# Optimization experiments

Measured on AMD Instinct MI355X. Metric: run time of the kernel, lower is better.

The kernel has to match this reference:

```python
import jax, jax.numpy as jnp
import numpy as np

N = 100          # num_objects
H = 128          # decoder_hidden
D = 128          # input_size (== H, required by the module's GRU linears)
REL = 7          # num_relative_features (use_3d=False)
E = N * (N - 1)  # fully-connected, no self loops
B = 32

_mask = ~np.eye(N, dtype=bool)
_SEND_NP, _RECV_NP = np.where(_mask)  # torch.where(~eye): rows=send, cols=recv
SEND = jnp.asarray(_SEND_NP, dtype=jnp.int32)
RECV = jnp.asarray(_RECV_NP, dtype=jnp.int32)


def setup_inputs() -> dict:
    key = jax.random.key(0)
    ks = jax.random.split(key, 34)
    def w(k, shape, scale=0.05):
        return jax.random.normal(k, shape, dtype=jnp.float32) * scale
    inp = {
        "inputs": jax.random.normal(ks[0], (B, N, D), jnp.float32),
        "edge_attr": jax.random.normal(ks[1], (B, E, REL + D), jnp.float32),
        "hidden": jax.random.normal(ks[2], (B, N, H), jnp.float32),
        # msg_mlp: Linear(2H,H) Tanh Linear(H,H) Tanh
        "msg_w1": w(ks[3], (2 * H, H)), "msg_b1": w(ks[4], (H,)),
        "msg_w2": w(ks[5], (H, H)),     "msg_b2": w(ks[6], (H,)),
        # present_msg_mlp: Linear(REL+D,H) ReLU Linear(H,H) ReLU
        "pm_w1": w(ks[7], (REL + D, H)), "pm_b1": w(ks[8], (H,)),
        "pm_w2": w(ks[9], (H, H)),       "pm_b2": w(ks[10], (H,)),
        # res_mlp: Linear(D,H) ReLU Linear(H,H) ReLU
        "res_w1": w(ks[11], (D, H)), "res_b1": w(ks[12], (H,)),
        "res_w2": w(ks[13], (H, H)), "res_b2": w(ks[14], (H,)),
        # GRU-style gates
        "ir_w": w(ks[15], (H, H)), "ir_b": w(ks[16], (H,)),
        "ii_w": w(ks[17], (H, H)), "ii_b": w(ks[18], (H,)),
        "in_w": w(ks[19], (H, H)), "in_b": w(ks[20], (H,)),
        "hr_w": w(ks[21], (H, H)),
        "hi_w": w(ks[22], (H, H)),
        "hh_w": w(ks[23], (H, H)),
        # out_mlp: Linear(H,H) ReLU Linear(H,H) ReLU Linear(H,D)
        "out_w1": w(ks[24], (H, H)), "out_b1": w(ks[25], (H,)),
        "out_w2": w(ks[26], (H, H)), "out_b2": w(ks[27], (H,)),
        "out_w3": w(ks[28], (H, D)), "out_b3": w(ks[29], (D,)),
    }
    return inp


def _scatter_mean(msgs, recv, num_nodes):
    # msgs: [B, E, H] -> [B, N, H], mean over incoming edges per node
    counts = jnp.zeros((num_nodes,), msgs.dtype).at[recv].add(1.0)
    summed = jnp.zeros((msgs.shape[0], num_nodes, msgs.shape[-1]), msgs.dtype)
    summed = summed.at[:, recv].add(msgs)
    return summed / counts[None, :, None]


def reference(inputs, edge_attr, hidden,
              msg_w1, msg_b1, msg_w2, msg_b2,
              pm_w1, pm_b1, pm_w2, pm_b2,
              res_w1, res_b1, res_w2, res_b2,
              ir_w, ir_b, ii_w, ii_b, in_w, in_b,
              hr_w, hi_w, hh_w,
              out_w1, out_b1, out_w2, out_b2, out_w3, out_b3):
    # gather hidden states along edges (dropout is identity: p=0 / eval)
    hm = jnp.concatenate([hidden[:, RECV], hidden[:, SEND]], axis=-1)  # [B,E,2H]
    hm = jnp.tanh(jnp.tanh(hm @ msg_w1 + msg_b1) @ msg_w2 + msg_b2)
    hidden_node = _scatter_mean(hm, RECV, N)                           # [B,N,H]

    pm = jax.nn.relu(jax.nn.relu(edge_attr @ pm_w1 + pm_b1) @ pm_w2 + pm_b2)
    present_node = _scatter_mean(pm, RECV, N)
    present_node = present_node + jax.nn.relu(
        jax.nn.relu(inputs @ res_w1 + res_b1) @ res_w2 + res_b2)

    r = jax.nn.sigmoid(present_node @ ir_w + ir_b + hidden_node @ hr_w)
    i = jax.nn.sigmoid(present_node @ ii_w + ii_b + hidden_node @ hi_w)
    n = jnp.tanh(present_node @ in_w + in_b + r * (hidden_node @ hh_w))
    hidden_new = (1.0 - i) * n + i * hidden

    pred = jax.nn.relu(hidden_new @ out_w1 + out_b1)
    pred = jax.nn.relu(pred @ out_w2 + out_b2)
    pred = pred @ out_w3 + out_b3
    return pred, hidden_new
```

## Files before the change

### kernel.cpp

```cpp
#include <hip/hip_runtime.h>

typedef unsigned short u16;
typedef unsigned int   u32;
typedef __attribute__((ext_vector_type(8))) short bf8;
typedef __attribute__((ext_vector_type(4))) float f4;

#define DF __device__ __forceinline__

DF float bf2f(u16 h){ u32 u = ((u32)h) << 16; float f; __builtin_memcpy(&f, &u, 4); return f; }
DF u16 f2bf(float f){ u32 u; __builtin_memcpy(&u, &f, 4); u = (u + 0x7FFFu + ((u >> 16) & 1u)) >> 16; return (u16)u; }
DF float fexp2(float x){ return __builtin_amdgcn_exp2f(x); }
DF float frcp (float x){ return __builtin_amdgcn_rcpf(x); }
DF float tanhF(float x){ float e = fexp2(2.8853900817779268f * x); return 1.0f - 2.0f * frcp(e + 1.0f); }
DF float sigF (float x){ return frcp(1.0f + fexp2(-1.4426950408889634f * x)); }
DF float4 ld4u(const float* p){ float4 v; __builtin_memcpy(&v, p, 16); return v; }
DF u32 cvtpk(float lo, float hi){ u32 r; asm("v_cvt_pk_bf16_f32 %0, %1, %2" : "=v"(r) : "v"(lo), "v"(hi)); return r; }

DF const bf8* fragp(const u16* packed, int w, int nt, int ks, int lane){
  return reinterpret_cast<const bf8*>(packed + (((w * 32 + nt * 4 + ks) * 64 + lane) * 8));
}
DF const bf8* fragp_pm1(const u16* packed, int nt, int ks, int lane){
  return reinterpret_cast<const bf8*>(packed + (((512 + nt * 5 + ks) * 64 + lane) * 8));
}

struct WPtrs { const float* p[16]; };

__global__ __launch_bounds__(256) void k_pack(WPtrs wp, u16* __restrict__ packed){
  int bi = blockIdx.x;
  int lane = threadIdx.x & 63, warp = threadIdx.x >> 6;
  if(bi == 16){
    const float* __restrict__ src = wp.p[14];
    u16* __restrict__ dst = packed + 512 * 64 * 8;
    for(int i = warp; i < 40; i += 4){
      int nt = i / 5, ks = i - nt * 5;
      int col = nt * 16 + (lane & 15);
      int kb  = ks * 32 + (lane >> 4) * 8;
      u16* o = dst + (i * 64 + lane) * 8;
      for(int j = 0; j < 8; j++){
        int row = kb + j;
        o[j] = (row < 135) ? f2bf(src[row * 128 + col]) : (u16)0;
      }
    }
    return;
  }
  const float* __restrict__ src = wp.p[bi];
  u16* __restrict__ dst = packed + bi * 32 * 64 * 8;
  for(int i = warp; i < 32; i += 4){
    int nt = i >> 2, ks = i & 3;
    int col = nt * 16 + (lane & 15);
    int kb  = ks * 32 + (lane >> 4) * 8;
    u16* o = dst + (i * 64 + lane) * 8;
    for(int j = 0; j < 8; j++) o[j] = f2bf(src[(kb + j) * 128 + col]);
  }
}

__global__ __launch_bounds__(512) void k_node_pre(
    const float* __restrict__ hidden, const float* __restrict__ inputs,
    const u16* __restrict__ packed,
    const float* __restrict__ res_b1, const float* __restrict__ res_b2,
    float* __restrict__ Ptop, float* __restrict__ Pbot, float* __restrict__ res2)
{
  __shared__ __align__(16) u16 hid[64 * 136];
  __shared__ __align__(16) u16 inp[64 * 136];
  __shared__ __align__(16) u16 t1s[64 * 136];
  int row0 = blockIdx.x * 64;
  int t = threadIdx.x, lane = t & 63, w = t >> 6;
  int lrow = lane & 15, lk = lane >> 4;
  for(int i = t; i < 64 * 128; i += 512){
    int rr = i >> 7, cc = i & 127;
    hid[rr * 136 + cc] = f2bf(hidden[(row0 + rr) * 128 + cc]);
    inp[rr * 136 + cc] = f2bf(inputs[(row0 + rr) * 128 + cc]);
  }
  bf8 f0[4], f1[4], f5[4], f6[4];
  #pragma unroll
  for(int k = 0; k < 4; k++){
    f0[k] = *fragp(packed, 0, w, k, lane);
    f1[k] = *fragp(packed, 1, w, k, lane);
    f5[k] = *fragp(packed, 5, w, k, lane);
    f6[k] = *fragp(packed, 6, w, k, lane);
  }
  int col = w * 16 + lrow;
  float rb1 = res_b1[col], rb2 = res_b2[col];
  __syncthreads();
  #pragma unroll
  for(int m = 0; m < 4; m++){
    bf8 a[4], a2[4];
    #pragma unroll
    for(int k = 0; k < 4; k++){
      a[k]  = *reinterpret_cast<const bf8*>(&hid[(m * 16 + lrow) * 136 + k * 32 + lk * 8]);
      a2[k] = *reinterpret_cast<const bf8*>(&inp[(m * 16 + lrow) * 136 + k * 32 + lk * 8]);
    }
    f4 c0 = {0.f,0.f,0.f,0.f}, c1 = {0.f,0.f,0.f,0.f}, c2 = {0.f,0.f,0.f,0.f};
    #pragma unroll
    for(int k = 0; k < 4; k++){
      c0 = __builtin_amdgcn_mfma_f32_16x16x32_bf16(a[k],  f0[k], c0, 0, 0, 0);
      c1 = __builtin_amdgcn_mfma_f32_16x16x32_bf16(a[k],  f1[k], c1, 0, 0, 0);
      c2 = __builtin_amdgcn_mfma_f32_16x16x32_bf16(a2[k], f5[k], c2, 0, 0, 0);
    }
    #pragma unroll
    for(int q = 0; q < 4; q++){
      int gr = row0 + m * 16 + lk * 4 + q;
      Ptop[gr * 128 + col] = c0[q];
      Pbot[gr * 128 + col] = c1[q];
      float v = c2[q] + rb1; v = v > 0.f ? v : 0.f;
      t1s[(m * 16 + lk * 4 + q) * 136 + col] = f2bf(v);
    }
  }
  __syncthreads();
  #pragma unroll
  for(int m = 0; m < 4; m++){
    bf8 a3[4];
    #pragma unroll
    for(int k = 0; k < 4; k++)
      a3[k] = *reinterpret_cast<const bf8*>(&t1s[(m * 16 + lrow) * 136 + k * 32 + lk * 8]);
    f4 c = {0.f,0.f,0.f,0.f};
    #pragma unroll
    for(int k = 0; k < 4; k++)
      c = __builtin_amdgcn_mfma_f32_16x16x32_bf16(a3[k], f6[k], c, 0, 0, 0);
    #pragma unroll
    for(int q = 0; q < 4; q++){
      float v = c[q] + rb2; v = v > 0.f ? v : 0.f;
      res2[(row0 + m * 16 + lk * 4 + q) * 128 + col] = v;
    }
  }
}

__global__ __launch_bounds__(256, 4) void k_edge(
    const float* __restrict__ EA,
    const float* __restrict__ Ptop, const float* __restrict__ Pbot,
    const float* __restrict__ msg_b1, const float* __restrict__ msg_b2,
    const float* __restrict__ pm_b1, const float* __restrict__ pm_b2,
    const u16* __restrict__ packed,
    float* __restrict__ hnode, float* __restrict__ pnode)
{
  __shared__ __align__(16) u16 bufA[112 * 128];
  __shared__ __align__(16) u16 tail[112 * 8];
  char* bb = (char*)bufA;
  char* tb = (char*)tail;
  int blk = blockIdx.x;
  int b = blk / 100, r = blk - b * 100;
  int t = threadIdx.x, lane = t & 63, w = t >> 6;
  int lrow = lane & 15, lk = lane >> 4;
  int n0 = 2 * w, n1 = 2 * w + 1;

  {
    for(int i = t; i < 99 * 16; i += 256){
      int row = i >> 4, g = i & 15;
      int s = row + (row >= r ? 1 : 0);
      int e = s * 99 + (r < s ? r : r - 1);
      const float* rp = EA + ((size_t)(b * 9900 + e)) * 135 + g * 8;
      float4 v0 = ld4u(rp), v1 = ld4u(rp + 4);
      u32 pk[4] = {cvtpk(v0.x, v0.y), cvtpk(v0.z, v0.w), cvtpk(v1.x, v1.y), cvtpk(v1.z, v1.w)};
      *reinterpret_cast<uint4*>(bb + row * 256 + ((g ^ (row & 7)) << 4)) = *reinterpret_cast<const uint4*>(pk);
    }
    for(int row = t; row < 99; row += 256){
      int s = row + (row >= r ? 1 : 0);
      int e = s * 99 + (r < s ? r : r - 1);
      const float* rp = EA + ((size_t)(b * 9900 + e)) * 135 + 128;
      float4 v0 = ld4u(rp);
      u32 pk[4] = {cvtpk(v0.x, v0.y), cvtpk(v0.z, v0.w), cvtpk(rp[4], rp[5]), cvtpk(rp[6], 0.f)};
      *reinterpret_cast<uint4*>(tb + row * 16) = *reinterpret_cast<const uint4*>(pk);
    }
    bf8 w1a[5], w1b[5];
    #pragma unroll
    for(int k = 0; k < 5; k++){ w1a[k] = *fragp_pm1(packed, n0, k, lane); w1b[k] = *fragp_pm1(packed, n1, k, lane); }
    float b1a = pm_b1[n0 * 16 + lrow], b1b = pm_b1[n1 * 16 + lrow];
    __syncthreads();

    f4 cA0[4], cA1[4];
    #pragma unroll
    for(int m = 0; m < 4; m++){
      int arow = m * 16 + lrow, sw = arow & 7;
      bf8 a[4];
      #pragma unroll
      for(int k = 0; k < 4; k++)
        a[k] = *reinterpret_cast<const bf8*>(bb + arow * 256 + (((k * 4 + lk) ^ sw) << 4));
      bf8 a4 = {0,0,0,0,0,0,0,0};
      if(lk == 0) a4 = *reinterpret_cast<const bf8*>(tb + arow * 16);
      f4 c0 = {0.f,0.f,0.f,0.f}, c1 = {0.f,0.f,0.f,0.f};
      #pragma unroll
      for(int k = 0; k < 4; k++){
        c0 = __builtin_amdgcn_mfma_f32_16x16x32_bf16(a[k], w1a[k], c0, 0, 0, 0);
        c1 = __builtin_amdgcn_mfma_f32_16x16x32_bf16(a[k], w1b[k], c1, 0, 0, 0);
      }
      c0 = __builtin_amdgcn_mfma_f32_16x16x32_bf16(a4, w1a[4], c0, 0, 0, 0);
      c1 = __builtin_amdgcn_mfma_f32_16x16x32_bf16(a4, w1b[4], c1, 0, 0, 0);
      cA0[m] = c0; cA1[m] = c1;
    }
    __syncthreads();

    #pragma unroll
    for(int m = 0; m < 4; m++){
      #pragma unroll
      for(int qp = 0; qp < 2; qp++){
        float v0 = cA0[m][2*qp]   + b1a; v0 = v0 > 0.f ? v0 : 0.f;
        float u0 = cA0[m][2*qp+1] + b1a; u0 = u0 > 0.f ? u0 : 0.f;
        float v1 = cA1[m][2*qp]   + b1b; v1 = v1 > 0.f ? v1 : 0.f;
        float u1 = cA1[m][2*qp+1] + b1b; u1 = u1 > 0.f ? u1 : 0.f;
        u32 p0 = cvtpk(v0, u0), p1 = cvtpk(v1, u1);
        int row0_ = m * 16 + lk * 4 + 2 * qp;
        int sw0 = (row0_ & 7) << 4, sw1 = ((row0_ + 1) & 7) << 4;
        *reinterpret_cast<u16*>(bb + row0_ * 256       + (((n0 * 16 + lrow) * 2) ^ sw0)) = (u16)p0;
        *reinterpret_cast<u16*>(bb + (row0_ + 1) * 256 + (((n0 * 16 + lrow) * 2) ^ sw1)) = (u16)(p0 >> 16);
        *reinterpret_cast<u16*>(bb + row0_ * 256       + (((n1 * 16 + lrow) * 2) ^ sw0)) = (u16)p1;
        *reinterpret_cast<u16*>(bb + (row0_ + 1) * 256 + (((n1 * 16 + lrow) * 2) ^ sw1)) = (u16)(p1 >> 16);
      }
    }
    f4 cB0[3], cB1[3];
    #pragma unroll
    for(int m = 0; m < 3; m++){
      int arow = (m + 4) * 16 + lrow, sw = arow & 7;
      bf8 a[4];
      #pragma unroll
      for(int k = 0; k < 4; k++)
        a[k] = *reinterpret_cast<const bf8*>(bb + arow * 256 + (((k * 4 + lk) ^ sw) << 4));
      bf8 a4 = {0,0,0,0,0,0,0,0};
      if(lk == 0) a4 = *reinterpret_cast<const bf8*>(tb + arow * 16);
      f4 c0 = {0.f,0.f,0.f,0.f}, c1 = {0.f,0.f,0.f,0.f};
      #pragma unroll
      for(int k = 0; k < 4; k++){
        c0 = __builtin_amdgcn_mfma_f32_16x16x32_bf16(a[k], w1a[k], c0, 0, 0, 0);
        c1 = __builtin_amdgcn_mfma_f32_16x16x32_bf16(a[k], w1b[k], c1, 0, 0, 0);
      }
      c0 = __builtin_amdgcn_mfma_f32_16x16x32_bf16(a4, w1a[4], c0, 0, 0, 0);
      c1 = __builtin_amdgcn_mfma_f32_16x16x32_bf16(a4, w1b[4], c1, 0, 0, 0);
      cB0[m] = c0; cB1[m] = c1;
    }
    __syncthreads();

    #pragma unroll
    for(int m = 0; m < 3; m++){
      #pragma unroll
      for(int qp = 0; qp < 2; qp++){
        float v0 = cB0[m][2*qp]   + b1a; v0 = v0 > 0.f ? v0 : 0.f;
        float u0 = cB0[m][2*qp+1] + b1a; u0 = u0 > 0.f ? u0 : 0.f;
        float v1 = cB1[m][2*qp]   + b1b; v1 = v1 > 0.f ? v1 : 0.f;
        float u1 = cB1[m][2*qp+1] + b1b; u1 = u1 > 0.f ? u1 : 0.f;
        u32 p0 = cvtpk(v0, u0), p1 = cvtpk(v1, u1);
        int row0_ = (m + 4) * 16 + lk * 4 + 2 * qp;
        int sw0 = (row0_ & 7) << 4, sw1 = ((row0_ + 1) & 7) << 4;
        *reinterpret_cast<u16*>(bb + row0_ * 256       + (((n0 * 16 + lrow) * 2) ^ sw0)) = (u16)p0;
        *reinterpret_cast<u16*>(bb + (row0_ + 1) * 256 + (((n0 * 16 + lrow) * 2) ^ sw1)) = (u16)(p0 >> 16);
        *reinterpret_cast<u16*>(bb + row0_ * 256       + (((n1 * 16 + lrow) * 2) ^ sw0)) = (u16)p1;
        *reinterpret_cast<u16*>(bb + (row0_ + 1) * 256 + (((n1 * 16 + lrow) * 2) ^ sw1)) = (u16)(p1 >> 16);
      }
    }
    __syncthreads();

    bf8 w2a[4], w2b[4];
    #pragma unroll
    for(int k = 0; k < 4; k++){ w2a[k] = *fragp(packed, 15, n0, k, lane); w2b[k] = *fragp(packed, 15, n1, k, lane); }
    float b2a = pm_b2[n0 * 16 + lrow], b2b = pm_b2[n1 * 16 + lrow];
    float acc0 = 0.f, acc1 = 0.f;
    #pragma unroll
    for(int m = 0; m < 7; m++){
      int arow = m * 16 + lrow, sw = arow & 7;
      bf8 a[4];
      #pragma unroll
      for(int k = 0; k < 4; k++)
        a[k] = *reinterpret_cast<const bf8*>(bb + arow * 256 + (((k * 4 + lk) ^ sw) << 4));
      f4 c0 = {0.f,0.f,0.f,0.f}, c1 = {0.f,0.f,0.f,0.f};
      #pragma unroll
      for(int k = 0; k < 4; k++){
        c0 = __builtin_amdgcn_mfma_f32_16x16x32_bf16(a[k], w2a[k], c0, 0, 0, 0);
        c1 = __builtin_amdgcn_mfma_f32_16x16x32_bf16(a[k], w2b[k], c1, 0, 0, 0);
      }
      #pragma unroll
      for(int q = 0; q < 4; q++){
        int rr = m * 16 + lk * 4 + q;
        if(rr < 99){
          float v0 = c0[q] + b2a; acc0 += (v0 > 0.f ? v0 : 0.f);
          float v1 = c1[q] + b2b; acc1 += (v1 > 0.f ? v1 : 0.f);
        }
      }
    }
    acc0 += __shfl_xor(acc0, 16); acc0 += __shfl_xor(acc0, 32);
    acc1 += __shfl_xor(acc1, 16); acc1 += __shfl_xor(acc1, 32);
    if(lane < 16){
      float* dst = pnode + ((size_t)b * 100 + r) * 128;
      dst[n0 * 16 + lane] = acc0 * (1.0f / 99.0f);
      dst[n1 * 16 + lane] = acc1 * (1.0f / 99.0f);
    }
  }
  __syncthreads();

  {
    bf8 w2a[4], w2b[4];
    #pragma unroll
    for(int k = 0; k < 4; k++){ w2a[k] = *fragp(packed, 13, n0, k, lane); w2b[k] = *fragp(packed, 13, n1, k, lane); }
    float b2a = msg_b2[n0 * 16 + lrow], b2b = msg_b2[n1 * 16 + lrow];
    int c4 = t & 31;
    float4 pt = *reinterpret_cast<const float4*>(Ptop + ((size_t)b * 100 + r) * 128 + c4 * 4);
    float4 mb = *reinterpret_cast<const float4*>(msg_b1 + c4 * 4);
    pt.x += mb.x; pt.y += mb.y; pt.z += mb.z; pt.w += mb.w;
    for(int row = t >> 5; row < 99; row += 8){
      int s = row + (row >= r ? 1 : 0);
      float4 v = *reinterpret_cast<const float4*>(Pbot + ((size_t)b * 100 + s) * 128 + c4 * 4);
      u32 pk[2] = {cvtpk(tanhF(pt.x + v.x), tanhF(pt.y + v.y)),
                   cvtpk(tanhF(pt.z + v.z), tanhF(pt.w + v.w))};
      *reinterpret_cast<uint2*>(bb + row * 256 + ((8 * c4) ^ ((row & 7) << 4))) = *reinterpret_cast<const uint2*>(pk);
    }
    __syncthreads();
    float acc0 = 0.f, acc1 = 0.f;
    #pragma unroll
    for(int m = 0; m < 7; m++){
      int arow = m * 16 + lrow, sw = arow & 7;
      bf8 a[4];
      #pragma unroll
      for(int k = 0; k < 4; k++)
        a[k] = *reinterpret_cast<const bf8*>(bb + arow * 256 + (((k * 4 + lk) ^ sw) << 4));
      f4 c0 = {0.f,0.f,0.f,0.f}, c1 = {0.f,0.f,0.f,0.f};
      #pragma unroll
      for(int k = 0; k < 4; k++){
        c0 = __builtin_amdgcn_mfma_f32_16x16x32_bf16(a[k], w2a[k], c0, 0, 0, 0);
        c1 = __builtin_amdgcn_mfma_f32_16x16x32_bf16(a[k], w2b[k], c1, 0, 0, 0);
      }
      #pragma unroll
      for(int q = 0; q < 4; q++){
        int rr = m * 16 + lk * 4 + q;
        if(rr < 99){
          acc0 += tanhF(c0[q] + b2a);
          acc1 += tanhF(c1[q] + b2b);
        }
      }
    }
    acc0 += __shfl_xor(acc0, 16); acc0 += __shfl_xor(acc0, 32);
    acc1 += __shfl_xor(acc1, 16); acc1 += __shfl_xor(acc1, 32);
    if(lane < 16){
      float* dst = hnode + ((size_t)b * 100 + r) * 128;
      dst[n0 * 16 + lane] = acc0 * (1.0f / 99.0f);
      dst[n1 * 16 + lane] = acc1 * (1.0f / 99.0f);
    }
  }
}

__global__ __launch_bounds__(512) void k_final(
    const float* __restrict__ hnode, const float* __restrict__ pnode,
    const float* __restrict__ res2, const float* __restrict__ hidden,
    const u16* __restrict__ packed,
    const float* __restrict__ ir_b, const float* __restrict__ ii_b, const float* __restrict__ in_b,
    const float* __restrict__ ob1, const float* __restrict__ ob2, const float* __restrict__ ob3,
    float* __restrict__ out_pred, float* __restrict__ out_hid)
{
  __shared__ __align__(16) u16 hn[64 * 136];
  __shared__ __align__(16) u16 pr[64 * 136];
  __shared__ __align__(16) u16 hw[64 * 136];
  int row0 = blockIdx.x * 64;
  int t = threadIdx.x, lane = t & 63, w = t >> 6;
  int lrow = lane & 15, lk = lane >> 4;
  for(int i = t; i < 64 * 128; i += 512){
    int rr = i >> 7, cc = i & 127;
    hn[rr * 136 + cc] = f2bf(hnode[(row0 + rr) * 128 + cc]);
    pr[rr * 136 + cc] = f2bf(pnode[(row0 + rr) * 128 + cc] + res2[(row0 + rr) * 128 + cc]);
  }
  int col = w * 16 + lrow;
  bf8 mhr[4], mhi[4], mhh[4], mir[4], mii[4], min_[4];
  #pragma unroll
  for(int k = 0; k < 4; k++){
    mhr[k]  = *fragp(packed, 2, w, k, lane);
    mhi[k]  = *fragp(packed, 3, w, k, lane);
    mhh[k]  = *fragp(packed, 4, w, k, lane);
    mir[k]  = *fragp(packed, 7, w, k, lane);
    mii[k]  = *fragp(packed, 8, w, k, lane);
    min_[k] = *fragp(packed, 9, w, k, lane);
  }
  float bir = ir_b[col], bii = ii_b[col], bin = in_b[col];
  __syncthreads();
  #pragma unroll
  for(int m = 0; m < 4; m++){
    bf8 a[4], p[4];
    #pragma unroll
    for(int k = 0; k < 4; k++){
      a[k] = *reinterpret_cast<const bf8*>(&hn[(m * 16 + lrow) * 136 + k * 32 + lk * 8]);
      p[k] = *reinterpret_cast<const bf8*>(&pr[(m * 16 + lrow) * 136 + k * 32 + lk * 8]);
    }
    f4 cR = {0.f,0.f,0.f,0.f}, cI = {0.f,0.f,0.f,0.f}, cN = {0.f,0.f,0.f,0.f};
    f4 dR = {0.f,0.f,0.f,0.f}, dI = {0.f,0.f,0.f,0.f}, dN = {0.f,0.f,0.f,0.f};
    #pragma unroll
    for(int k = 0; k < 4; k++){
      cR = __builtin_amdgcn_mfma_f32_16x16x32_bf16(a[k], mhr[k],  cR, 0, 0, 0);
      cI = __builtin_amdgcn_mfma_f32_16x16x32_bf16(a[k], mhi[k],  cI, 0, 0, 0);
      cN = __builtin_amdgcn_mfma_f32_16x16x32_bf16(a[k], mhh[k],  cN, 0, 0, 0);
      dR = __builtin_amdgcn_mfma_f32_16x16x32_bf16(p[k], mir[k],  dR, 0, 0, 0);
      dI = __builtin_amdgcn_mfma_f32_16x16x32_bf16(p[k], mii[k],  dI, 0, 0, 0);
      dN = __builtin_amdgcn_mfma_f32_16x16x32_bf16(p[k], min_[k], dN, 0, 0, 0);
    }
    #pragma unroll
    for(int q = 0; q < 4; q++){
      int gr = row0 + m * 16 + lk * 4 + q;
      float rv = sigF(dR[q] + bir + cR[q]);
      float iv = sigF(dI[q] + bii + cI[q]);
      float nv = tanhF(dN[q] + bin + rv * cN[q]);
      float hold = hidden[gr * 128 + col];
      float hnew = (1.f - iv) * nv + iv * hold;
      out_hid[gr * 128 + col] = hnew;
      hw[(m * 16 + lk * 4 + q) * 136 + col] = f2bf(hnew);
    }
  }
  __syncthreads();
  {
    bf8 m10[4];
    #pragma unroll
    for(int k = 0; k < 4; k++) m10[k] = *fragp(packed, 10, w, k, lane);
    float bb = ob1[col];
    #pragma unroll
    for(int m = 0; m < 4; m++){
      f4 c = {0.f,0.f,0.f,0.f};
      #pragma unroll
      for(int k = 0; k < 4; k++){
        bf8 a = *reinterpret_cast<const bf8*>(&hw[(m * 16 + lrow) * 136 + k * 32 + lk * 8]);
        c = __builtin_amdgcn_mfma_f32_16x16x32_bf16(a, m10[k], c, 0, 0, 0);
      }
      #pragma unroll
      for(int q = 0; q < 4; q++){
        float v = c[q] + bb; v = v > 0.f ? v : 0.f;
        hn[(m * 16 + lk * 4 + q) * 136 + col] = f2bf(v);
      }
    }
  }
  __syncthreads();
  {
    bf8 m11[4];
    #pragma unroll
    for(int k = 0; k < 4; k++) m11[k] = *fragp(packed, 11, w, k, lane);
    float bb = ob2[col];
    #pragma unroll
    for(int m = 0; m < 4; m++){
      f4 c = {0.f,0.f,0.f,0.f};
      #pragma unroll
      for(int k = 0; k < 4; k++){
        bf8 a = *reinterpret_cast<const bf8*>(&hn[(m * 16 + lrow) * 136 + k * 32 + lk * 8]);
        c = __builtin_amdgcn_mfma_f32_16x16x32_bf16(a, m11[k], c, 0, 0, 0);
      }
      #pragma unroll
      for(int q = 0; q < 4; q++){
        float v = c[q] + bb; v = v > 0.f ? v : 0.f;
        pr[(m * 16 + lk * 4 + q) * 136 + col] = f2bf(v);
      }
    }
  }
  __syncthreads();
  {
    bf8 m12[4];
    #pragma unroll
    for(int k = 0; k < 4; k++) m12[k] = *fragp(packed, 12, w, k, lane);
    float bb = ob3[col];
    #pragma unroll
    for(int m = 0; m < 4; m++){
      f4 c = {0.f,0.f,0.f,0.f};
      #pragma unroll
      for(int k = 0; k < 4; k++){
        bf8 a = *reinterpret_cast<const bf8*>(&pr[(m * 16 + lrow) * 136 + k * 32 + lk * 8]);
        c = __builtin_amdgcn_mfma_f32_16x16x32_bf16(a, m12[k], c, 0, 0, 0);
      }
      #pragma unroll
      for(int q = 0; q < 4; q++)
        out_pred[(row0 + m * 16 + lk * 4 + q) * 128 + col] = c[q] + bb;
    }
  }
}

extern "C" void kernel_launch(void* const* d_in, const int* in_sizes, int n_in,
                              void* d_out, int out_size, void* d_ws, size_t ws_size,
                              hipStream_t stream)
{
  const float* inputs = (const float*)d_in[0];
  const float* edge   = (const float*)d_in[1];
  const float* hidden = (const float*)d_in[2];
  const float* msg_w1 = (const float*)d_in[3];
  const float* msg_b1 = (const float*)d_in[4];
  const float* msg_w2 = (const float*)d_in[5];
  const float* msg_b2 = (const float*)d_in[6];
  const float* pm_w1  = (const float*)d_in[7];
  const float* pm_b1  = (const float*)d_in[8];
  const float* pm_w2  = (const float*)d_in[9];
  const float* pm_b2  = (const float*)d_in[10];
  const float* res_w1 = (const float*)d_in[11];
  const float* res_b1 = (const float*)d_in[12];
  const float* res_w2 = (const float*)d_in[13];
  const float* res_b2 = (const float*)d_in[14];
  const float* ir_w = (const float*)d_in[15]; const float* ir_b = (const float*)d_in[16];
  const float* ii_w = (const float*)d_in[17]; const float* ii_b = (const float*)d_in[18];
  const float* in_w = (const float*)d_in[19]; const float* in_b = (const float*)d_in[20];
  const float* hr_w = (const float*)d_in[21];
  const float* hi_w = (const float*)d_in[22];
  const float* hh_w = (const float*)d_in[23];
  const float* out_w1 = (const float*)d_in[24]; const float* out_b1 = (const float*)d_in[25];
  const float* out_w2 = (const float*)d_in[26]; const float* out_b2 = (const float*)d_in[27];
  const float* out_w3 = (const float*)d_in[28]; const float* out_b3 = (const float*)d_in[29];

  char* ws = (char*)d_ws;
  u16*   packed = (u16*)ws;
  float* Ptop   = (float*)(ws + (1 << 20));
  float* Pbot   = (float*)(ws + (1 << 20) + 1 * 1638400);
  float* res2   = (float*)(ws + (1 << 20) + 2 * 1638400);
  float* hnode  = (float*)(ws + (1 << 20) + 3 * 1638400);
  float* pnode  = (float*)(ws + (1 << 20) + 4 * 1638400);

  WPtrs wp;
  wp.p[0]  = msg_w1;
  wp.p[1]  = msg_w1 + 128 * 128;
  wp.p[2]  = hr_w;  wp.p[3]  = hi_w;  wp.p[4]  = hh_w;
  wp.p[5]  = res_w1; wp.p[6] = res_w2;
  wp.p[7]  = ir_w;  wp.p[8]  = ii_w;  wp.p[9]  = in_w;
  wp.p[10] = out_w1; wp.p[11] = out_w2; wp.p[12] = out_w3;
  wp.p[13] = msg_w2; wp.p[14] = pm_w1; wp.p[15] = pm_w2;

  k_pack<<<17, 256, 0, stream>>>(wp, packed);
  k_node_pre<<<50, 512, 0, stream>>>(hidden, inputs, packed, res_b1, res_b2, Ptop, Pbot, res2);
  k_edge<<<3200, 256, 0, stream>>>(edge, Ptop, Pbot, msg_b1, msg_b2, pm_b1, pm_b2,
                                   packed, hnode, pnode);
  float* outp = (float*)d_out;
  k_final<<<50, 512, 0, stream>>>(hnode, pnode, res2, hidden, packed,
                                  ir_b, ii_b, in_b, out_b1, out_b2, out_b3,
                                  outp, outp + 32 * 100 * 128);
}
```

Baseline: 118.7 us.

## Double edge-kernel waves to 8 with one output tile each, reduce register pressure

The edge kernel now runs 512 threads per block, so each of 8 waves owns a single 16-column output tile instead of two. The hidden-state staging loop stride is widened to match. This halves per-wave accumulator and weight-fragment registers and doubles the waves available to hide load latency on the edge-attribute gather. Weight fragments in the node kernels are also loaded closer to their point of use to shorten register live ranges. The trade-off is more waves per block competing at barriers, and fewer resident blocks per CU under the (512,4) bound.

```diff
diff --git a/kernel.cpp b/kernel.cpp
--- a/kernel.cpp
+++ b/kernel.cpp
@@ -71,61 +71,67 @@
     hid[rr * 136 + cc] = f2bf(hidden[(row0 + rr) * 128 + cc]);
     inp[rr * 136 + cc] = f2bf(inputs[(row0 + rr) * 128 + cc]);
   }
-  bf8 f0[4], f1[4], f5[4], f6[4];
-  #pragma unroll
-  for(int k = 0; k < 4; k++){
-    f0[k] = *fragp(packed, 0, w, k, lane);
-    f1[k] = *fragp(packed, 1, w, k, lane);
-    f5[k] = *fragp(packed, 5, w, k, lane);
-    f6[k] = *fragp(packed, 6, w, k, lane);
-  }
   int col = w * 16 + lrow;
   float rb1 = res_b1[col], rb2 = res_b2[col];
   __syncthreads();
-  #pragma unroll
-  for(int m = 0; m < 4; m++){
-    bf8 a[4], a2[4];
+  {
+    bf8 f0[4], f1[4], f5[4];
     #pragma unroll
     for(int k = 0; k < 4; k++){
-      a[k]  = *reinterpret_cast<const bf8*>(&hid[(m * 16 + lrow) * 136 + k * 32 + lk * 8]);
-      a2[k] = *reinterpret_cast<const bf8*>(&inp[(m * 16 + lrow) * 136 + k * 32 + lk * 8]);
-    }
-    f4 c0 = {0.f,0.f,0.f,0.f}, c1 = {0.f,0.f,0.f,0.f}, c2 = {0.f,0.f,0.f,0.f};
-    #pragma unroll
-    for(int k = 0; k < 4; k++){
-      c0 = __builtin_amdgcn_mfma_f32_16x16x32_bf16(a[k],  f0[k], c0, 0, 0, 0);
-      c1 = __builtin_amdgcn_mfma_f32_16x16x32_bf16(a[k],  f1[k], c1, 0, 0, 0);
-      c2 = __builtin_amdgcn_mfma_f32_16x16x32_bf16(a2[k], f5[k], c2, 0, 0, 0);
-    }
-    #pragma unroll
-    for(int q = 0; q < 4; q++){
-      int gr = row0 + m * 16 + lk * 4 + q;
-      Ptop[gr * 128 + col] = c0[q];
-      Pbot[gr * 128 + col] = c1[q];
-      float v = c2[q] + rb1; v = v > 0.f ? v : 0.f;
-      t1s[(m * 16 + lk * 4 + q) * 136 + col] = f2bf(v);
-    }
-  }
-  __syncthreads();
-  #pragma unroll
-  for(int m = 0; m < 4; m++){
-    bf8 a3[4];
-    #pragma unroll
-    for(int k = 0; k < 4; k++)
-      a3[k] = *reinterpret_cast<const bf8*>(&t1s[(m * 16 + lrow) * 136 + k * 32 + lk * 8]);
-    f4 c = {0.f,0.f,0.f,0.f};
-    #pragma unroll
-    for(int k = 0; k < 4; k++)
-      c = __builtin_amdgcn_mfma_f32_16x16x32_bf16(a3[k], f6[k], c, 0, 0, 0);
-    #pragma unroll
-    for(int q = 0; q < 4; q++){
-      float v = c[q] + rb2; v = v > 0.f ? v : 0.f;
-      res2[(row0 + m * 16 + lk * 4 + q) * 128 + col] = v;
-    }
-  }
-}
-
-__global__ __launch_bounds__(256, 4) void k_edge(
+      f0[k] = *fragp(packed, 0, w, k, lane);
+      f1[k] = *fragp(packed, 1, w, k, lane);
+      f5[k] = *fragp(packed, 5, w, k, lane);
+    }
+    #pragma unroll
+    for(int m = 0; m < 4; m++){
+      bf8 a[4], a2[4];
+      #pragma unroll
+      for(int k = 0; k < 4; k++){
+        a[k]  = *reinterpret_cast<const bf8*>(&hid[(m * 16 + lrow) * 136 + k * 32 + lk * 8]);
+        a2[k] = *reinterpret_cast<const bf8*>(&inp[(m * 16 + lrow) * 136 + k * 32 + lk * 8]);
+      }
+      f4 c0 = {0.f,0.f,0.f,0.f}, c1 = {0.f,0.f,0.f,0.f}, c2 = {0.f,0.f,0.f,0.f};
+      #pragma unroll
+      for(int k = 0; k < 4; k++){
+        c0 = __builtin_amdgcn_mfma_f32_16x16x32_bf16(a[k],  f0[k], c0, 0, 0, 0);
+        c1 = __builtin_amdgcn_mfma_f32_16x16x32_bf16(a[k],  f1[k], c1, 0, 0, 0);
+        c2 = __builtin_amdgcn_mfma_f32_16x16x32_bf16(a2[k], f5[k], c2, 0, 0, 0);
+      }
+      #pragma unroll
+      for(int q = 0; q < 4; q++){
+        int gr = row0 + m * 16 + lk * 4 + q;
+        Ptop[gr * 128 + col] = c0[q];
+        Pbot[gr * 128 + col] = c1[q];
+        float v = c2[q] + rb1; v = v > 0.f ? v : 0.f;
+        t1s[(m * 16 + lk * 4 + q) * 136 + col] = f2bf(v);
+      }
+    }
+  }
+  __syncthreads();
+  {
+    bf8 f6[4];
+    #pragma unroll
+    for(int k = 0; k < 4; k++) f6[k] = *fragp(packed, 6, w, k, lane);
+    #pragma unroll
+    for(int m = 0; m < 4; m++){
+      bf8 a3[4];
+      #pragma unroll
+      for(int k = 0; k < 4; k++)
+        a3[k] = *reinterpret_cast<const bf8*>(&t1s[(m * 16 + lrow) * 136 + k * 32 + lk * 8]);
+      f4 c = {0.f,0.f,0.f,0.f};
+      #pragma unroll
+      for(int k = 0; k < 4; k++)
+        c = __builtin_amdgcn_mfma_f32_16x16x32_bf16(a3[k], f6[k], c, 0, 0, 0);
+      #pragma unroll
+      for(int q = 0; q < 4; q++){
+        float v = c[q] + rb2; v = v > 0.f ? v : 0.f;
+        res2[(row0 + m * 16 + lk * 4 + q) * 128 + col] = v;
+      }
+    }
+  }
+}
+
+__global__ __launch_bounds__(512, 4) void k_edge(
     const float* __restrict__ EA,
     const float* __restrict__ Ptop, const float* __restrict__ Pbot,
     const float* __restrict__ msg_b1, const float* __restrict__ msg_b2,
@@ -141,10 +147,9 @@
   int b = blk / 100, r = blk - b * 100;
   int t = threadIdx.x, lane = t & 63, w = t >> 6;
   int lrow = lane & 15, lk = lane >> 4;
-  int n0 = 2 * w, n1 = 2 * w + 1;
-
-  {
-    for(int i = t; i < 99 * 16; i += 256){
+
+  {
+    for(int i = t; i < 99 * 16; i += 512){
       int row = i >> 4, g = i & 15;
       int s = row + (row >= r ? 1 : 0);
       int e = s * 99 + (r < s ? r : r - 1);
@@ -153,7 +158,7 @@
       u32 pk[4] = {cvtpk(v0.x, v0.y), cvtpk(v0.z, v0.w), cvtpk(v1.x, v1.y), cvtpk(v1.z, v1.w)};
       *reinterpret_cast<uint4*>(bb + row * 256 + ((g ^ (row & 7)) << 4)) = *reinterpret_cast<const uint4*>(pk);
     }
-    for(int row = t; row < 99; row += 256){
+    for(int row = t; row < 99; row += 512){
       int s = row + (row >= r ? 1 : 0);
       int e = s * 99 + (r < s ? r : r - 1);
       const float* rp = EA + ((size_t)(b * 9900 + e)) * 135 + 128;
@@ -161,13 +166,14 @@
       u32 pk[4] = {cvtpk(v0.x, v0.y), cvtpk(v0.z, v0.w), cvtpk(rp[4], rp[5]), cvtpk(rp[6], 0.f)};
       *reinterpret_cast<uint4*>(tb + row * 16) = *reinterpret_cast<const uint4*>(pk);
     }
-    bf8 w1a[5], w1b[5];
-    #pragma unroll
-    for(int k = 0; k < 5; k++){ w1a[k] = *fragp_pm1(packed, n0, k, lane); w1b[k] = *fragp_pm1(packed, n1, k, lane); }
-    float b1a = pm_b1[n0 * 16 + lrow], b1b = pm_b1[n1 * 16 + lrow];
+    bf8 w1[5];
+    #pragma unroll
+    for(int k = 0; k < 5; k++) w1[k] = *fragp_pm1(packed, w, k, lane);
+    asm volatile("" : "+v"(w1[0]), "+v"(w1[1]), "+v"(w1[2]), "+v"(w1[3]), "+v"(w1[4]));
+    float b1 = pm_b1[w * 16 + lrow];
     __syncthreads();
 
-    f4 cA0[4], cA1[4];
+    f4 cA[4];
     #pragma unroll
     for(int m = 0; m < 4; m++){
       int arow = m * 16 + lrow, sw = arow & 7;
@@ -177,15 +183,12 @@
         a[k] = *reinterpret_cast<const bf8*>(bb + arow * 256 + (((k * 4 + lk) ^ sw) << 4));
       bf8 a4 = {0,0,0,0,0,0,0,0};
       if(lk == 0) a4 = *reinterpret_cast<const bf8*>(tb + arow * 16);
-      f4 c0 = {0.f,0.f,0.f,0.f}, c1 = {0.f,0.f,0.f,0.f};
-      #pragma unroll
-      for(int k = 0; k < 4; k++){
-        c0 = __builtin_amdgcn_mfma_f32_16x16x32_bf16(a[k], w1a[k], c0, 0, 0, 0);
-        c1 = __builtin_amdgcn_mfma_f32_16x16x32_bf16(a[k], w1b[k], c1, 0, 0, 0);
-      }
-      c0 = __builtin_amdgcn_mfma_f32_16x16x32_bf16(a4, w1a[4], c0, 0, 0, 0);
-      c1 = __builtin_amdgcn_mfma_f32_16x16x32_bf16(a4, w1b[4], c1, 0, 0, 0);
-      cA0[m] = c0; cA1[m] = c1;
+      f4 c = {0.f,0.f,0.f,0.f};
+      #pragma unroll
+      for(int k = 0; k < 4; k++)
+        c = __builtin_amdgcn_mfma_f32_16x16x32_bf16(a[k], w1[k], c, 0, 0, 0);
+      c = __builtin_amdgcn_mfma_f32_16x16x32_bf16(a4, w1[4], c, 0, 0, 0);
+      cA[m] = c;
     }
     __syncthreads();
 
@@ -193,20 +196,16 @@
     for(int m = 0; m < 4; m++){
       #pragma unroll
       for(int qp = 0; qp < 2; qp++){
-        float v0 = cA0[m][2*qp]   + b1a; v0 = v0 > 0.f ? v0 : 0.f;
-        float u0 = cA0[m][2*qp+1] + b1a; u0 = u0 > 0.f ? u0 : 0.f;
-        float v1 = cA1[m][2*qp]   + b1b; v1 = v1 > 0.f ? v1 : 0.f;
-        float u1 = cA1[m][2*qp+1] + b1b; u1 = u1 > 0.f ? u1 : 0.f;
-        u32 p0 = cvtpk(v0, u0), p1 = cvtpk(v1, u1);
+        float v0 = cA[m][2*qp]   + b1; v0 = v0 > 0.f ? v0 : 0.f;
+        float u0 = cA[m][2*qp+1] + b1; u0 = u0 > 0.f ? u0 : 0.f;
+        u32 p0 = cvtpk(v0, u0);
         int row0_ = m * 16 + lk * 4 + 2 * qp;
         int sw0 = (row0_ & 7) << 4, sw1 = ((row0_ + 1) & 7) << 4;
-        *reinterpret_cast<u16*>(bb + row0_ * 256       + (((n0 * 16 + lrow) * 2) ^ sw0)) = (u16)p0;
-        *reinterpret_cast<u16*>(bb + (row0_ + 1) * 256 + (((n0 * 16 + lrow) * 2) ^ sw1)) = (u16)(p0 >> 16);
-        *reinterpret_cast<u16*>(bb + row0_ * 256       + (((n1 * 16 + lrow) * 2) ^ sw0)) = (u16)p1;
-        *reinterpret_cast<u16*>(bb + (row0_ + 1) * 256 + (((n1 * 16 + lrow) * 2) ^ sw1)) = (u16)(p1 >> 16);
-      }
-    }
-    f4 cB0[3], cB1[3];
+        *reinterpret_cast<u16*>(bb + row0_ * 256       + (((w * 16 + lrow) * 2) ^ sw0)) = (u16)p0;
+        *reinterpret_cast<u16*>(bb + (row0_ + 1) * 256 + (((w * 16 + lrow) * 2) ^ sw1)) = (u16)(p0 >> 16);
+      }
+    }
+    f4 cB[3];
     #pragma unroll
     for(int m = 0; m < 3; m++){
       int arow = (m + 4) * 16 + lrow, sw = arow & 7;
@@ -216,15 +215,12 @@
         a[k] = *reinterpret_cast<const bf8*>(bb + arow * 256 + (((k * 4 + lk) ^ sw) << 4));
       bf8 a4 = {0,0,0,0,0,0,0,0};
       if(lk == 0) a4 = *reinterpret_cast<const bf8*>(tb + arow * 16);
-      f4 c0 = {0.f,0.f,0.f,0.f}, c1 = {0.f,0.f,0.f,0.f};
-      #pragma unroll
-      for(int k = 0; k < 4; k++){
-        c0 = __builtin_amdgcn_mfma_f32_16x16x32_bf16(a[k], w1a[k], c0, 0, 0, 0);
-        c1 = __builtin_amdgcn_mfma_f32_16x16x32_bf16(a[k], w1b[k], c1, 0, 0, 0);
-      }
-      c0 = __builtin_amdgcn_mfma_f32_16x16x32_bf16(a4, w1a[4], c0, 0, 0, 0);
-      c1 = __builtin_amdgcn_mfma_f32_16x16x32_bf16(a4, w1b[4], c1, 0, 0, 0);
-      cB0[m] = c0; cB1[m] = c1;
+      f4 c = {0.f,0.f,0.f,0.f};
+      #pragma unroll
+      for(int k = 0; k < 4; k++)
+        c = __builtin_amdgcn_mfma_f32_16x16x32_bf16(a[k], w1[k], c, 0, 0, 0);
+      c = __builtin_amdgcn_mfma_f32_16x16x32_bf16(a4, w1[4], c, 0, 0, 0);
+      cB[m] = c;
     }
     __syncthreads();
 
@@ -232,26 +228,22 @@
     for(int m = 0; m < 3; m++){
       #pragma unroll
       for(int qp = 0; qp < 2; qp++){
-        float v0 = cB0[m][2*qp]   + b1a; v0 = v0 > 0.f ? v0 : 0.f;
-        float u0 = cB0[m][2*qp+1] + b1a; u0 = u0 > 0.f ? u0 : 0.f;
-        float v1 = cB1[m][2*qp]   + b1b; v1 = v1 > 0.f ? v1 : 0.f;
-        float u1 = cB1[m][2*qp+1] + b1b; u1 = u1 > 0.f ? u1 : 0.f;
-        u32 p0 = cvtpk(v0, u0), p1 = cvtpk(v1, u1);
+        float v0 = cB[m][2*qp]   + b1; v0 = v0 > 0.f ? v0 : 0.f;
+        float u0 = cB[m][2*qp+1] + b1; u0 = u0 > 0.f ? u0 : 0.f;
+        u32 p0 = cvtpk(v0, u0);
         int row0_ = (m + 4) * 16 + lk * 4 + 2 * qp;
         int sw0 = (row0_ & 7) << 4, sw1 = ((row0_ + 1) & 7) << 4;
-        *reinterpret_cast<u16*>(bb + row0_ * 256       + (((n0 * 16 + lrow) * 2) ^ sw0)) = (u16)p0;
-        *reinterpret_cast<u16*>(bb + (row0_ + 1) * 256 + (((n0 * 16 + lrow) * 2) ^ sw1)) = (u16)(p0 >> 16);
-        *reinterpret_cast<u16*>(bb + row0_ * 256       + (((n1 * 16 + lrow) * 2) ^ sw0)) = (u16)p1;
-        *reinterpret_cast<u16*>(bb + (row0_ + 1) * 256 + (((n1 * 16 + lrow) * 2) ^ sw1)) = (u16)(p1 >> 16);
+        *reinterpret_cast<u16*>(bb + row0_ * 256       + (((w * 16 + lrow) * 2) ^ sw0)) = (u16)p0;
+        *reinterpret_cast<u16*>(bb + (row0_ + 1) * 256 + (((w * 16 + lrow) * 2) ^ sw1)) = (u16)(p0 >> 16);
       }
     }
     __syncthreads();
 
-    bf8 w2a[4], w2b[4];
-    #pragma unroll
-    for(int k = 0; k < 4; k++){ w2a[k] = *fragp(packed, 15, n0, k, lane); w2b[k] = *fragp(packed, 15, n1, k, lane); }
-    float b2a = pm_b2[n0 * 16 + lrow], b2b = pm_b2[n1 * 16 + lrow];
-    float acc0 = 0.f, acc1 = 0.f;
+    bf8 w2[4];
+    #pragma unroll
+    for(int k = 0; k < 4; k++) w2[k] = *fragp(packed, 15, w, k, lane);
+    float b2 = pm_b2[w * 16 + lrow];
+    float acc = 0.f;
     #pragma unroll
     for(int m = 0; m < 7; m++){
       int arow = m * 16 + lrow, sw = arow & 7;
@@ -259,41 +251,31 @@
       #pragma unroll
       for(int k = 0; k < 4; k++)
         a[k] = *reinterpret_cast<const bf8*>(bb + arow * 256 + (((k * 4 + lk) ^ sw) << 4));
-      f4 c0 = {0.f,0.f,0.f,0.f}, c1 = {0.f,0.f,0.f,0.f};
-      #pragma unroll
-      for(int k = 0; k < 4; k++){
-        c0 = __builtin_amdgcn_mfma_f32_16x16x32_bf16(a[k], w2a[k], c0, 0, 0, 0);
-        c1 = __builtin_amdgcn_mfma_f32_16x16x32_bf16(a[k], w2b[k], c1, 0, 0, 0);
-      }
+      f4 c = {0.f,0.f,0.f,0.f};
+      #pragma unroll
+      for(int k = 0; k < 4; k++)
+        c = __builtin_amdgcn_mfma_f32_16x16x32_bf16(a[k], w2[k], c, 0, 0, 0);
       #pragma unroll
       for(int q = 0; q < 4; q++){
         int rr = m * 16 + lk * 4 + q;
-        if(rr < 99){
-          float v0 = c0[q] + b2a; acc0 += (v0 > 0.f ? v0 : 0.f);
-          float v1 = c1[q] + b2b; acc1 += (v1 > 0.f ? v1 : 0.f);
-        }
-      }
-    }
-    acc0 += __shfl_xor(acc0, 16); acc0 += __shfl_xor(acc0, 32);
-    acc1 += __shfl_xor(acc1, 16); acc1 += __shfl_xor(acc1, 32);
-    if(lane < 16){
-      float* dst = pnode + ((size_t)b * 100 + r) * 128;
-      dst[n0 * 16 + lane] = acc0 * (1.0f / 99.0f);
-      dst[n1 * 16 + lane] = acc1 * (1.0f / 99.0f);
-    }
-  }
-  __syncthreads();
-
-  {
-    bf8 w2a[4], w2b[4];
-    #pragma unroll
-    for(int k = 0; k < 4; k++){ w2a[k] = *fragp(packed, 13, n0, k, lane); w2b[k] = *fragp(packed, 13, n1, k, lane); }
-    float b2a = msg_b2[n0 * 16 + lrow], b2b = msg_b2[n1 * 16 + lrow];
+        if(rr < 99){ float v = c[q] + b2; acc += (v > 0.f ? v : 0.f); }
+      }
+    }
+    acc += __shfl_xor(acc, 16); acc += __shfl_xor(acc, 32);
+    if(lane < 16) pnode[((size_t)b * 100 + r) * 128 + w * 16 + lane] = acc * (1.0f / 99.0f);
+  }
+  __syncthreads();
+
+  {
+    bf8 w2[4];
+    #pragma unroll
+    for(int k = 0; k < 4; k++) w2[k] = *fragp(packed, 13, w, k, lane);
+    float b2 = msg_b2[w * 16 + lrow];
     int c4 = t & 31;
     float4 pt = *reinterpret_cast<const float4*>(Ptop + ((size_t)b * 100 + r) * 128 + c4 * 4);
     float4 mb = *reinterpret_cast<const float4*>(msg_b1 + c4 * 4);
     pt.x += mb.x; pt.y += mb.y; pt.z += mb.z; pt.w += mb.w;
-    for(int row = t >> 5; row < 99; row += 8){
+    for(int row = t >> 5; row < 99; row += 16){
       int s = row + (row >= r ? 1 : 0);
       float4 v = *reinterpret_cast<const float4*>(Pbot + ((size_t)b * 100 + s) * 128 + c4 * 4);
       u32 pk[2] = {cvtpk(tanhF(pt.x + v.x), tanhF(pt.y + v.y)),
@@ -301,7 +283,7 @@
       *reinterpret_cast<uint2*>(bb + row * 256 + ((8 * c4) ^ ((row & 7) << 4))) = *reinterpret_cast<const uint2*>(pk);
     }
     __syncthreads();
-    float acc0 = 0.f, acc1 = 0.f;
+    float acc = 0.f;
     #pragma unroll
     for(int m = 0; m < 7; m++){
       int arow = m * 16 + lrow, sw = arow & 7;
@@ -309,28 +291,18 @@
       #pragma unroll
       for(int k = 0; k < 4; k++)
         a[k] = *reinterpret_cast<const bf8*>(bb + arow * 256 + (((k * 4 + lk) ^ sw) << 4));
-      f4 c0 = {0.f,0.f,0.f,0.f}, c1 = {0.f,0.f,0.f,0.f};
-      #pragma unroll
-      for(int k = 0; k < 4; k++){
-        c0 = __builtin_amdgcn_mfma_f32_16x16x32_bf16(a[k], w2a[k], c0, 0, 0, 0);
-        c1 = __builtin_amdgcn_mfma_f32_16x16x32_bf16(a[k], w2b[k], c1, 0, 0, 0);
-      }
+      f4 c = {0.f,0.f,0.f,0.f};
+      #pragma unroll
+      for(int k = 0; k < 4; k++)
+        c = __builtin_amdgcn_mfma_f32_16x16x32_bf16(a[k], w2[k], c, 0, 0, 0);
       #pragma unroll
       for(int q = 0; q < 4; q++){
         int rr = m * 16 + lk * 4 + q;
-        if(rr < 99){
-          acc0 += tanhF(c0[q] + b2a);
-          acc1 += tanhF(c1[q] + b2b);
-        }
-      }
-    }
-    acc0 += __shfl_xor(acc0, 16); acc0 += __shfl_xor(acc0, 32);
-    acc1 += __shfl_xor(acc1, 16); acc1 += __shfl_xor(acc1, 32);
-    if(lane < 16){
-      float* dst = hnode + ((size_t)b * 100 + r) * 128;
-      dst[n0 * 16 + lane] = acc0 * (1.0f / 99.0f);
-      dst[n1 * 16 + lane] = acc1 * (1.0f / 99.0f);
-    }
+        if(rr < 99) acc += tanhF(c[q] + b2);
+      }
+    }
+    acc += __shfl_xor(acc, 16); acc += __shfl_xor(acc, 32);
+    if(lane < 16) hnode[((size_t)b * 100 + r) * 128 + w * 16 + lane] = acc * (1.0f / 99.0f);
   }
 }
 
@@ -354,16 +326,6 @@
     pr[rr * 136 + cc] = f2bf(pnode[(row0 + rr) * 128 + cc] + res2[(row0 + rr) * 128 + cc]);
   }
   int col = w * 16 + lrow;
-  bf8 mhr[4], mhi[4], mhh[4], mir[4], mii[4], min_[4];
-  #pragma unroll
-  for(int k = 0; k < 4; k++){
-    mhr[k]  = *fragp(packed, 2, w, k, lane);
-    mhi[k]  = *fragp(packed, 3, w, k, lane);
-    mhh[k]  = *fragp(packed, 4, w, k, lane);
-    mir[k]  = *fragp(packed, 7, w, k, lane);
-    mii[k]  = *fragp(packed, 8, w, k, lane);
-    min_[k] = *fragp(packed, 9, w, k, lane);
-  }
   float bir = ir_b[col], bii = ii_b[col], bin = in_b[col];
   __syncthreads();
   #pragma unroll
@@ -378,12 +340,12 @@
     f4 dR = {0.f,0.f,0.f,0.f}, dI = {0.f,0.f,0.f,0.f}, dN = {0.f,0.f,0.f,0.f};
     #pragma unroll
     for(int k = 0; k < 4; k++){
-      cR = __builtin_amdgcn_mfma_f32_16x16x32_bf16(a[k], mhr[k],  cR, 0, 0, 0);
-      cI = __builtin_amdgcn_mfma_f32_16x16x32_bf16(a[k], mhi[k],  cI, 0, 0, 0);
-      cN = __builtin_amdgcn_mfma_f32_16x16x32_bf16(a[k], mhh[k],  cN, 0, 0, 0);
-      dR = __builtin_amdgcn_mfma_f32_16x16x32_bf16(p[k], mir[k],  dR, 0, 0, 0);
-      dI = __builtin_amdgcn_mfma_f32_16x16x32_bf16(p[k], mii[k],  dI, 0, 0, 0);
-      dN = __builtin_amdgcn_mfma_f32_16x16x32_bf16(p[k], min_[k], dN, 0, 0, 0);
+      cR = __builtin_amdgcn_mfma_f32_16x16x32_bf16(a[k], *fragp(packed, 2, w, k, lane), cR, 0, 0, 0);
+      cI = __builtin_amdgcn_mfma_f32_16x16x32_bf16(a[k], *fragp(packed, 3, w, k, lane), cI, 0, 0, 0);
+      cN = __builtin_amdgcn_mfma_f32_16x16x32_bf16(a[k], *fragp(packed, 4, w, k, lane), cN, 0, 0, 0);
+      dR = __builtin_amdgcn_mfma_f32_16x16x32_bf16(p[k], *fragp(packed, 7, w, k, lane), dR, 0, 0, 0);
+      dI = __builtin_amdgcn_mfma_f32_16x16x32_bf16(p[k], *fragp(packed, 8, w, k, lane), dI, 0, 0, 0);
+      dN = __builtin_amdgcn_mfma_f32_16x16x32_bf16(p[k], *fragp(packed, 9, w, k, lane), dN, 0, 0, 0);
     }
     #pragma unroll
     for(int q = 0; q < 4; q++){
@@ -508,7 +470,7 @@
 
   k_pack<<<17, 256, 0, stream>>>(wp, packed);
   k_node_pre<<<50, 512, 0, stream>>>(hidden, inputs, packed, res_b1, res_b2, Ptop, Pbot, res2);
-  k_edge<<<3200, 256, 0, stream>>>(edge, Ptop, Pbot, msg_b1, msg_b2, pm_b1, pm_b2,
+  k_edge<<<3200, 512, 0, stream>>>(edge, Ptop, Pbot, msg_b1, msg_b2, pm_b1, pm_b2,
                                    packed, hnode, pnode);
   float* outp = (float*)d_out;
   k_final<<<50, 512, 0, stream>>>(hnode, pnode, res2, hidden, packed,
```

Result: slower. 129.6 us (+9.1%).
